# Kernel tuning notes

Hardware: AMD Instinct MI355X
Metric: run time of the kernel (lower is better)

Reference implementation:

```python
import jax, jax.numpy as jnp
import numpy as np

OUT_FEATURES = 4096
IN_FEATURES = 11008
VECTOR_DIM = 8
N_CODES = 32768

def setup_inputs() -> dict:
    key = jax.random.key(0)
    k1, k2, k3, k4 = jax.random.split(key, 4)
    n_vectors = OUT_FEATURES * IN_FEATURES // VECTOR_DIM
    x = jax.random.normal(k1, (2, 2048, IN_FEATURES), dtype=jnp.float32)
    indices = jax.random.randint(k2, (n_vectors,), 0, N_CODES, dtype=jnp.int32)
    codebook = jax.random.normal(k3, (N_CODES, VECTOR_DIM), dtype=jnp.float32)
    scales = jax.random.uniform(k4, (OUT_FEATURES, 1), dtype=jnp.float32)
    return {"x": x, "indices": indices, "codebook": codebook, "scales": scales}

def reference(x, indices, codebook, scales):
    # Dequantize: gather codebook vectors, reshape to [out, in], apply per-row scale
    w = codebook[indices].reshape(OUT_FEATURES, IN_FEATURES) * scales
    # F.linear(x, w) == x @ w.T
    return jnp.einsum('bsi,oi->bso', x, w)
```

## Files before the change

kernel.cpp:

```cpp
#include <hip/hip_runtime.h>
#include <cstdint>
#include <cstddef>

#define OUT_F 4096
#define IN_F  11008
#define VECD  8
#define NVEC  (OUT_F * IN_F / VECD)
#define VPR   (IN_F / VECD)
#define M_DIM 4096
#define N_DIM OUT_F
#define K_DIM IN_F

typedef __attribute__((ext_vector_type(4))) float f32x4;
typedef __attribute__((ext_vector_type(8))) __bf16 bf16x8;
typedef __attribute__((ext_vector_type(4))) unsigned int u32x4;

__device__ inline unsigned short f2bf(float f) {
  union { float f; unsigned int u; } v; v.f = f;
  unsigned int u = v.u;
  unsigned int r = u + 0x7FFFu + ((u >> 16) & 1u);
  return (unsigned short)(r >> 16);
}

__global__ __launch_bounds__(256) void dequant_cast_kernel(
    const float* __restrict__ x, const int* __restrict__ indices,
    const float* __restrict__ cb, const float* __restrict__ scales,
    unsigned short* __restrict__ xb, unsigned short* __restrict__ wb) {
  int v = blockIdx.x * 256 + threadIdx.x;
  if (v >= NVEC) return;

  int id = indices[v];
  int o  = v / VPR;
  float s = scales[o];

  const f32x4* c = (const f32x4*)(cb + (size_t)id * VECD);
  f32x4 c0 = c[0], c1 = c[1];
  u32x4 w;
  w.x = (unsigned)f2bf(c0.x * s) | ((unsigned)f2bf(c0.y * s) << 16);
  w.y = (unsigned)f2bf(c0.z * s) | ((unsigned)f2bf(c0.w * s) << 16);
  w.z = (unsigned)f2bf(c1.x * s) | ((unsigned)f2bf(c1.y * s) << 16);
  w.w = (unsigned)f2bf(c1.z * s) | ((unsigned)f2bf(c1.w * s) << 16);
  *(u32x4*)(wb + (size_t)v * 8) = w;

  const f32x4* xp = (const f32x4*)(x + (size_t)v * 8);
  f32x4 x0 = xp[0], x1 = xp[1];
  u32x4 q;
  q.x = (unsigned)f2bf(x0.x) | ((unsigned)f2bf(x0.y) << 16);
  q.y = (unsigned)f2bf(x0.z) | ((unsigned)f2bf(x0.w) << 16);
  q.z = (unsigned)f2bf(x1.x) | ((unsigned)f2bf(x1.y) << 16);
  q.w = (unsigned)f2bf(x1.z) | ((unsigned)f2bf(x1.w) << 16);
  *(u32x4*)(xb + (size_t)v * 8) = q;
}

#define GLD16(g, l)                                                     \
  __builtin_amdgcn_global_load_lds(                                     \
      (const __attribute__((address_space(1))) void*)(g),               \
      (__attribute__((address_space(3))) void*)(l), 16, 0, 0)

__global__ __launch_bounds__(512, 2) void gemm_bt_kernel(
    const unsigned short* __restrict__ A,
    const unsigned short* __restrict__ B,
    float* __restrict__ C) {
  extern __shared__ unsigned short SMEM[];
  unsigned short* SA = SMEM;
  unsigned short* SB = SMEM + 3 * 8192;

  const int tid  = threadIdx.x;
  const int bm   = blockIdx.x >> 4;
  const int bn   = blockIdx.x & 15;
  const int lane = tid & 63;
  const int wave = tid >> 6;
  const int wm   = (wave & 1) * 128;
  const int wn   = (wave >> 1) * 64;
  const int lrow = lane & 15;
  const int kgrp = lane >> 4;
  const int kslot = (kgrp ^ ((lrow >> 1) & 3)) * 8;

  const int srow = tid >> 2;
  const int cg   = (tid & 3) ^ ((srow >> 1) & 3);
  const unsigned short* a0 = A + (size_t)(bm * 256 + srow) * K_DIM + cg * 8;
  const unsigned short* a1 = a0 + (size_t)128 * K_DIM;
  const unsigned short* b0 = B + (size_t)(bn * 256 + srow) * K_DIM + cg * 8;
  const unsigned short* b1 = b0 + (size_t)128 * K_DIM;
  const int l0 = tid * 8;
  const int l1 = 4096 + tid * 8;

#define STAGE(pbuf, kf)                                   \
  do {                                                    \
    GLD16(a0 + (kf), &SA[(pbuf) * 8192 + l0]);            \
    GLD16(a1 + (kf), &SA[(pbuf) * 8192 + l1]);            \
    GLD16(b0 + (kf), &SB[(pbuf) * 8192 + l0]);            \
    GLD16(b1 + (kf), &SB[(pbuf) * 8192 + l1]);            \
  } while (0)

  f32x4 acc[8][4];
#pragma unroll
  for (int i = 0; i < 8; i++)
#pragma unroll
    for (int j = 0; j < 4; j++) acc[i][j] = f32x4{0.f, 0.f, 0.f, 0.f};

  STAGE(0, 0);
  STAGE(1, 32);
  int cbuf = 0, pbuf = 2;

  for (int k0 = 0; k0 < K_DIM; k0 += 32) {
    asm volatile("s_waitcnt vmcnt(4)\n\ts_barrier" ::: "memory");

    int kf = k0 + 64;
    if (kf > K_DIM - 32) kf = K_DIM - 32;
    STAGE(pbuf, kf);

    bf16x8 af[8], bfr[4];
#pragma unroll
    for (int i = 0; i < 8; i++)
      af[i] = *(const bf16x8*)&SA[cbuf * 8192 + (wm + i * 16 + lrow) * 32 + kslot];
#pragma unroll
    for (int j = 0; j < 4; j++)
      bfr[j] = *(const bf16x8*)&SB[cbuf * 8192 + (wn + j * 16 + lrow) * 32 + kslot];

#pragma unroll
    for (int i = 0; i < 8; i++)
#pragma unroll
      for (int j = 0; j < 4; j++)
        acc[i][j] = __builtin_amdgcn_mfma_f32_16x16x32_bf16(
            af[i], bfr[j], acc[i][j], 0, 0, 0);

    cbuf = (cbuf == 2) ? 0 : cbuf + 1;
    pbuf = (pbuf == 2) ? 0 : pbuf + 1;
  }
#undef STAGE

#pragma unroll
  for (int i = 0; i < 8; i++) {
    const int row0 = bm * 256 + wm + i * 16 + kgrp * 4;
#pragma unroll
    for (int j = 0; j < 4; j++) {
      const int col = bn * 256 + wn + j * 16 + lrow;
#pragma unroll
      for (int r = 0; r < 4; r++)
        C[(size_t)(row0 + r) * N_DIM + col] = acc[i][j][r];
    }
  }
}

__global__ __launch_bounds__(256) void naive_kernel(
    const float* __restrict__ x, const int* __restrict__ indices,
    const float* __restrict__ cb, const float* __restrict__ scales,
    float* __restrict__ out) {
  int n = blockIdx.x * 256 + threadIdx.x;
  int m = blockIdx.y;
  if (n >= N_DIM) return;
  float s = scales[n];
  const float* xr = x + (size_t)m * IN_F;
  const int* ir = indices + (size_t)n * VPR;
  float acc = 0.f;
  for (int v = 0; v < VPR; v++) {
    int id = ir[v];
    const float* c = cb + (size_t)id * 8;
#pragma unroll
    for (int e = 0; e < 8; e++) acc += xr[v * 8 + e] * c[e];
  }
  out[(size_t)m * N_DIM + n] = acc * s;
}

extern "C" void kernel_launch(void* const* d_in, const int* in_sizes, int n_in,
                              void* d_out, int out_size, void* d_ws, size_t ws_size,
                              hipStream_t stream) {
  const float* x       = (const float*)d_in[0];
  const int*   indices = (const int*)d_in[1];
  const float* cb      = (const float*)d_in[2];
  const float* scales  = (const float*)d_in[3];
  float* out = (float*)d_out;

  const size_t xb_elems = (size_t)M_DIM * K_DIM;
  const size_t wb_elems = (size_t)N_DIM * K_DIM;
  const size_t need = (xb_elems + wb_elems) * sizeof(unsigned short);

  if (ws_size >= need) {
    unsigned short* xb = (unsigned short*)d_ws;
    unsigned short* wb = xb + xb_elems;
    dequant_cast_kernel<<<NVEC / 256, 256, 0, stream>>>(x, indices, cb, scales,
                                                        xb, wb);
    gemm_bt_kernel<<<(M_DIM / 256) * (N_DIM / 256), 512, 6 * 8192 * 2, stream>>>(
        xb, wb, out);
  } else {
    naive_kernel<<<dim3(N_DIM / 256, M_DIM), 256, 0, stream>>>(x, indices, cb,
                                                               scales, out);
  }
}
```

Before: 636.7 us.

## Split GEMM k-step into two phases interleaving loads, MFMA and priority hints

Each k-iteration of the bf16 GEMM main loop is split into two halves. Each half issues its share of LDS fragment reads and global-to-LDS prefetches (A then B), then runs 16 MFMAs under raised wave priority with s_setprio. Extra barriers sit between the phases so the waves stay in lockstep, in the style of ping-pong scheduling meant to overlap memory issue with matrix math. The extra barriers and waitcnts add sync overhead and could serialize work if the waves do not interleave well.

```diff
diff --git a/kernel.cpp b/kernel.cpp
--- a/kernel.cpp
+++ b/kernel.cpp
@@ -85,10 +85,13 @@
   const int l0 = tid * 8;
   const int l1 = 4096 + tid * 8;
 
-#define STAGE(pbuf, kf)                                   \
+#define STAGE_A(pbuf, kf)                                 \
   do {                                                    \
     GLD16(a0 + (kf), &SA[(pbuf) * 8192 + l0]);            \
     GLD16(a1 + (kf), &SA[(pbuf) * 8192 + l1]);            \
+  } while (0)
+#define STAGE_B(pbuf, kf)                                 \
+  do {                                                    \
     GLD16(b0 + (kf), &SB[(pbuf) * 8192 + l0]);            \
     GLD16(b1 + (kf), &SB[(pbuf) * 8192 + l1]);            \
   } while (0)
@@ -99,36 +102,61 @@
 #pragma unroll
     for (int j = 0; j < 4; j++) acc[i][j] = f32x4{0.f, 0.f, 0.f, 0.f};
 
-  STAGE(0, 0);
-  STAGE(1, 32);
+  STAGE_A(0, 0);
+  STAGE_B(0, 0);
+  STAGE_A(1, 32);
+  STAGE_B(1, 32);
+  asm volatile("s_waitcnt vmcnt(4)\n\ts_barrier" ::: "memory");
   int cbuf = 0, pbuf = 2;
 
   for (int k0 = 0; k0 < K_DIM; k0 += 32) {
-    asm volatile("s_waitcnt vmcnt(4)\n\ts_barrier" ::: "memory");
-
     int kf = k0 + 64;
     if (kf > K_DIM - 32) kf = K_DIM - 32;
-    STAGE(pbuf, kf);
 
     bf16x8 af[8], bfr[4];
-#pragma unroll
-    for (int i = 0; i < 8; i++)
+
+#pragma unroll
+    for (int i = 0; i < 4; i++)
       af[i] = *(const bf16x8*)&SA[cbuf * 8192 + (wm + i * 16 + lrow) * 32 + kslot];
 #pragma unroll
     for (int j = 0; j < 4; j++)
       bfr[j] = *(const bf16x8*)&SB[cbuf * 8192 + (wn + j * 16 + lrow) * 32 + kslot];
-
-#pragma unroll
-    for (int i = 0; i < 8; i++)
+    STAGE_A(pbuf, kf);
+
+    __builtin_amdgcn_s_barrier();
+    asm volatile("s_waitcnt lgkmcnt(0)" ::: "memory");
+    __builtin_amdgcn_s_setprio(1);
+#pragma unroll
+    for (int i = 0; i < 4; i++)
 #pragma unroll
       for (int j = 0; j < 4; j++)
         acc[i][j] = __builtin_amdgcn_mfma_f32_16x16x32_bf16(
             af[i], bfr[j], acc[i][j], 0, 0, 0);
+    __builtin_amdgcn_s_setprio(0);
+    __builtin_amdgcn_s_barrier();
+
+#pragma unroll
+    for (int i = 4; i < 8; i++)
+      af[i] = *(const bf16x8*)&SA[cbuf * 8192 + (wm + i * 16 + lrow) * 32 + kslot];
+    STAGE_B(pbuf, kf);
+
+    __builtin_amdgcn_s_barrier();
+    asm volatile("s_waitcnt lgkmcnt(0)" ::: "memory");
+    __builtin_amdgcn_s_setprio(1);
+#pragma unroll
+    for (int i = 4; i < 8; i++)
+#pragma unroll
+      for (int j = 0; j < 4; j++)
+        acc[i][j] = __builtin_amdgcn_mfma_f32_16x16x32_bf16(
+            af[i], bfr[j], acc[i][j], 0, 0, 0);
+    __builtin_amdgcn_s_setprio(0);
+    asm volatile("s_waitcnt vmcnt(4)\n\ts_barrier" ::: "memory");
 
     cbuf = (cbuf == 2) ? 0 : cbuf + 1;
     pbuf = (pbuf == 2) ? 0 : pbuf + 1;
   }
-#undef STAGE
+#undef STAGE_A
+#undef STAGE_B
 
 #pragma unroll
   for (int i = 0; i < 8; i++) {
```

Result: slower. 666.2 us (+4.6%).

## Pre-cast codebook to bf16 and move per-row scale into GEMM epilogue

Applied to the files above, without the earlier changes.

Adds a small kernel that converts the codebook to bf16 once, so the dequant kernel gathers 16-byte bf16 codewords instead of 32-byte fp32 ones and does no scale multiply or conversion. The per-output-row scale is now applied in the GEMM epilogue, since scaling a row of W commutes with the matmul. This shrinks gather traffic and ALU work in the dequant pass at the cost of one extra tiny launch. Rounding changes slightly because the scale is now applied after bf16 accumulation rather than before the cast.

```diff
diff --git a/kernel.cpp b/kernel.cpp
--- a/kernel.cpp
+++ b/kernel.cpp
@@ -7,6 +7,7 @@
 #define VECD  8
 #define NVEC  (OUT_F * IN_F / VECD)
 #define VPR   (IN_F / VECD)
+#define NCODES 32768
 #define M_DIM 4096
 #define N_DIM OUT_F
 #define K_DIM IN_F
@@ -22,24 +23,29 @@
   return (unsigned short)(r >> 16);
 }
 
+__global__ __launch_bounds__(256) void cbcast_kernel(
+    const float* __restrict__ cb, unsigned short* __restrict__ cbb) {
+  int i = blockIdx.x * 256 + threadIdx.x;
+  if (i >= NCODES) return;
+  const f32x4* c = (const f32x4*)(cb + (size_t)i * VECD);
+  f32x4 c0 = c[0], c1 = c[1];
+  u32x4 w;
+  w.x = (unsigned)f2bf(c0.x) | ((unsigned)f2bf(c0.y) << 16);
+  w.y = (unsigned)f2bf(c0.z) | ((unsigned)f2bf(c0.w) << 16);
+  w.z = (unsigned)f2bf(c1.x) | ((unsigned)f2bf(c1.y) << 16);
+  w.w = (unsigned)f2bf(c1.z) | ((unsigned)f2bf(c1.w) << 16);
+  *(u32x4*)(cbb + (size_t)i * 8) = w;
+}
+
 __global__ __launch_bounds__(256) void dequant_cast_kernel(
     const float* __restrict__ x, const int* __restrict__ indices,
-    const float* __restrict__ cb, const float* __restrict__ scales,
-    unsigned short* __restrict__ xb, unsigned short* __restrict__ wb) {
+    const unsigned short* __restrict__ cbb, unsigned short* __restrict__ xb,
+    unsigned short* __restrict__ wb) {
   int v = blockIdx.x * 256 + threadIdx.x;
   if (v >= NVEC) return;
 
   int id = indices[v];
-  int o  = v / VPR;
-  float s = scales[o];
-
-  const f32x4* c = (const f32x4*)(cb + (size_t)id * VECD);
-  f32x4 c0 = c[0], c1 = c[1];
-  u32x4 w;
-  w.x = (unsigned)f2bf(c0.x * s) | ((unsigned)f2bf(c0.y * s) << 16);
-  w.y = (unsigned)f2bf(c0.z * s) | ((unsigned)f2bf(c0.w * s) << 16);
-  w.z = (unsigned)f2bf(c1.x * s) | ((unsigned)f2bf(c1.y * s) << 16);
-  w.w = (unsigned)f2bf(c1.z * s) | ((unsigned)f2bf(c1.w * s) << 16);
+  u32x4 w = *(const u32x4*)(cbb + (size_t)id * 8);
   *(u32x4*)(wb + (size_t)v * 8) = w;
 
   const f32x4* xp = (const f32x4*)(x + (size_t)v * 8);
@@ -60,6 +66,7 @@
 __global__ __launch_bounds__(512, 2) void gemm_bt_kernel(
     const unsigned short* __restrict__ A,
     const unsigned short* __restrict__ B,
+    const float* __restrict__ S,
     float* __restrict__ C) {
   extern __shared__ unsigned short SMEM[];
   unsigned short* SA = SMEM;
@@ -130,6 +137,11 @@
   }
 #undef STAGE
 
+  float sj[4];
+#pragma unroll
+  for (int j = 0; j < 4; j++)
+    sj[j] = S[bn * 256 + wn + j * 16 + lrow];
+
 #pragma unroll
   for (int i = 0; i < 8; i++) {
     const int row0 = bm * 256 + wm + i * 16 + kgrp * 4;
@@ -138,7 +150,7 @@
       const int col = bn * 256 + wn + j * 16 + lrow;
 #pragma unroll
       for (int r = 0; r < 4; r++)
-        C[(size_t)(row0 + r) * N_DIM + col] = acc[i][j][r];
+        C[(size_t)(row0 + r) * N_DIM + col] = acc[i][j][r] * sj[j];
     }
   }
 }
@@ -172,17 +184,20 @@
   const float* scales  = (const float*)d_in[3];
   float* out = (float*)d_out;
 
-  const size_t xb_elems = (size_t)M_DIM * K_DIM;
-  const size_t wb_elems = (size_t)N_DIM * K_DIM;
-  const size_t need = (xb_elems + wb_elems) * sizeof(unsigned short);
+  const size_t xb_elems  = (size_t)M_DIM * K_DIM;
+  const size_t wb_elems  = (size_t)N_DIM * K_DIM;
+  const size_t cbb_elems = (size_t)NCODES * VECD;
+  const size_t need =
+      (xb_elems + wb_elems + cbb_elems) * sizeof(unsigned short);
 
   if (ws_size >= need) {
-    unsigned short* xb = (unsigned short*)d_ws;
-    unsigned short* wb = xb + xb_elems;
-    dequant_cast_kernel<<<NVEC / 256, 256, 0, stream>>>(x, indices, cb, scales,
-                                                        xb, wb);
+    unsigned short* xb  = (unsigned short*)d_ws;
+    unsigned short* wb  = xb + xb_elems;
+    unsigned short* cbb = wb + wb_elems;
+    cbcast_kernel<<<NCODES / 256, 256, 0, stream>>>(cb, cbb);
+    dequant_cast_kernel<<<NVEC / 256, 256, 0, stream>>>(x, indices, cbb, xb, wb);
     gemm_bt_kernel<<<(M_DIM / 256) * (N_DIM / 256), 512, 6 * 8192 * 2, stream>>>(
-        xb, wb, out);
+        xb, wb, scales, out);
   } else {
     naive_kernel<<<dim3(N_DIM / 256, M_DIM), 256, 0, stream>>>(x, indices, cb,
                                                                scales, out);
```

New measurement: 638.6 us. Within noise of the previous version (+0.3%).
